# Kernel optimization log

Hardware: AMD Instinct MI355X
Metric: run time of the kernel (lower is better)

The kernel has to match this reference:

```python
import jax, jax.numpy as jnp
import numpy as np

B, LQ, LK, D = 8, 2048, 2048, 128

def setup_inputs() -> dict:
    key = jax.random.key(0)
    k1, k2, k3, k4 = jax.random.split(key, 4)
    return {
        "query": jax.random.normal(k1, (B, LQ, D), dtype=jnp.float32),
        "key": jax.random.normal(k2, (B, LK, D), dtype=jnp.float32),
        "value": jax.random.normal(k3, (B, LK, D), dtype=jnp.float32),
        "scale_factor": jax.random.normal(k4, (B, LQ, LK), dtype=jnp.float32),
    }

def reference(query, key, value, scale_factor):
    # qk: [B, LQ, LK]
    qk = jnp.einsum("bqd,bkd->bqk", query, key)
    probs = jax.nn.softmax(qk * scale_factor, axis=-1)
    # dropout_p = 0.0 -> identity
    return jnp.einsum("bqk,bkd->bqd", probs, value)
```

## Files before the change

### kernel.cpp

```cpp
#include <hip/hip_runtime.h>
#include <hip/hip_bf16.h>


typedef float          f32x4 __attribute__((ext_vector_type(4)));
typedef short          s16x8 __attribute__((ext_vector_type(8)));
typedef unsigned int   u32x4 __attribute__((ext_vector_type(4)));
typedef unsigned short u16x4 __attribute__((ext_vector_type(4)));

#define LOG2E 1.4426950408889634f

__device__ __forceinline__ float fast_exp2(float x) {
#if __has_builtin(__builtin_amdgcn_exp2f)
    return __builtin_amdgcn_exp2f(x);
#else
    return exp2f(x);
#endif
}

__device__ __forceinline__ unsigned short f2bf(float x) {
    return __builtin_bit_cast(unsigned short, __float2bfloat16(x));
}
__device__ __forceinline__ float bf2f(unsigned short u) {
    return __bfloat162float(__builtin_bit_cast(__hip_bfloat16, u));
}

__global__ void prep(const float* __restrict__ q,
                     const float* __restrict__ k,
                     const float* __restrict__ v,
                     unsigned short* __restrict__ qh,
                     unsigned short* __restrict__ ql,
                     unsigned short* __restrict__ kh,
                     unsigned short* __restrict__ kl,
                     unsigned short* __restrict__ vt) {
    __shared__ unsigned short tile[64 * 132];
    const int bb  = blockIdx.x;
    const int tid = threadIdx.x;

    if (bb < 4096) {
        const bool isq = bb < 2048;
        const float* src = isq ? q : k;
        unsigned short* hi = isq ? qh : kh;
        unsigned short* lo = isq ? ql : kl;
        const int i = (isq ? bb : bb - 2048) * 256 + tid;
        const float4 val = ((const float4*)src)[i];
        float f[4] = {val.x, val.y, val.z, val.w};
        u16x4 h, l;
#pragma unroll
        for (int j = 0; j < 4; ++j) {
            unsigned short hb = f2bf(f[j]);
            h[j] = hb;
            l[j] = f2bf(f[j] - bf2f(hb));
        }
        ((u16x4*)hi)[i] = h;
        ((u16x4*)lo)[i] = l;
        return;
    }

    const int tb = bb - 4096;
    const int b  = tb & 7;
    const int k0 = (tb >> 3) * 64;
#pragma unroll
    for (int p = 0; p < 8; ++p) {
        int idx  = p * 256 + tid;
        int kk   = idx >> 5;
        int dblk = idx & 31;
        float4 val = ((const float4*)v)[((b * 2048 + k0 + kk) * 128 + dblk * 4) >> 2];
        u16x4 t4;
        t4[0] = f2bf(val.x); t4[1] = f2bf(val.y);
        t4[2] = f2bf(val.z); t4[3] = f2bf(val.w);
        *(u16x4*)&tile[kk * 132 + dblk * 4] = t4;
    }
    __syncthreads();
#pragma unroll
    for (int p = 0; p < 4; ++p) {
        int idx = p * 256 + tid;
        int d   = idx >> 3;
        int k8  = idx & 7;
        u16x4 a, c;
#pragma unroll
        for (int j = 0; j < 4; ++j) a[j] = tile[(k8 * 8 + j) * 132 + d];
#pragma unroll
        for (int j = 0; j < 4; ++j) c[j] = tile[(k8 * 8 + 4 + j) * 132 + d];
        unsigned short* outp = vt + (b * 128 + d) * 2048 + k0 + k8 * 8;
        *(u16x4*)outp       = a;
        *(u16x4*)(outp + 4) = c;
    }
}

#define KHS 136
#define VTS 72

template <int KSPLIT>
__global__ __launch_bounds__(256, 3)
void flash_fwd(const unsigned short* __restrict__ qh_g,
               const unsigned short* __restrict__ ql_g,
               const unsigned short* __restrict__ kh_g,
               const unsigned short* __restrict__ kl_g,
               const unsigned short* __restrict__ vt_g,
               const float* __restrict__ scale_g,
               float* __restrict__ opart,
               float* __restrict__ mpart,
               float* __restrict__ lpart) {
    __shared__ unsigned short lds_kh[64 * KHS];
    __shared__ unsigned short lds_kl[64 * KHS];
    __shared__ unsigned short lds_vt[128 * VTS];

    const int tid  = threadIdx.x;
    const int wave = tid >> 6;
    const int lane = tid & 63;
    const int c    = lane & 15;
    const int g    = lane >> 4;

    const int bid   = blockIdx.x;
    const int b     = bid & 7;
    const int qt    = (bid >> 3) & 31;
    const int ks    = bid >> 8;
    const int q0    = qt * 64;

    const int PER   = (32 + KSPLIT - 1) / KSPLIT;
    const int kt0   = ks * PER;
    const int NIT   = min(PER, 32 - kt0);
    const int kbase = kt0 * 64;

    const int srow = tid >> 4, sc8 = tid & 15;
    const int sdv  = tid >> 3, sk8 = tid & 7;

    const int rc = 8 * (c >> 2) + (c & 3);

    s16x8 qh[4], ql[4];
    {
        const int qrow = b * 2048 + q0 + wave * 16 + c;
#pragma unroll
        for (int kstep = 0; kstep < 4; ++kstep) {
            int idx = qrow * 16 + kstep * 4 + g;
            qh[kstep] = __builtin_bit_cast(s16x8, ((const u32x4*)qh_g)[idx]);
            ql[kstep] = __builtin_bit_cast(s16x8, ((const u32x4*)ql_g)[idx]);
        }
    }

    f32x4 oacc[8];
#pragma unroll
    for (int t = 0; t < 8; ++t) oacc[t] = (f32x4){0.f, 0.f, 0.f, 0.f};
    float m2 = -INFINITY, ln = 0.f;

    u32x4 pk[4], pl[4], pv[4];
    float4 scn[4];
    const size_t scb = (size_t)(b * 2048 + q0 + wave * 16 + c) * 2048 + 8 * g;

    {
        const int k0 = kbase;
#pragma unroll
        for (int p = 0; p < 4; ++p) {
            int gidx = (b * 2048 + k0 + p * 16 + srow) * 16 + sc8;
            pk[p] = ((const u32x4*)kh_g)[gidx];
            pl[p] = ((const u32x4*)kl_g)[gidx];
            int vidx = (b * 128 + p * 32 + sdv) * 256 + (k0 >> 3) + sk8;
            pv[p] = ((const u32x4*)vt_g)[vidx];
        }
        scn[0] = *(const float4*)&scale_g[scb + k0 + 0];
        scn[1] = *(const float4*)&scale_g[scb + k0 + 32];
        scn[2] = *(const float4*)&scale_g[scb + k0 + 4];
        scn[3] = *(const float4*)&scale_g[scb + k0 + 36];
    }

    for (int kc = 0; kc < NIT; ++kc) {
        const int k0 = kbase + kc * 64;

        __syncthreads();
#pragma unroll
        for (int p = 0; p < 4; ++p) {
            *(u32x4*)&lds_kh[(p * 16 + srow) * KHS + sc8 * 8] = pk[p];
            *(u32x4*)&lds_kl[(p * 16 + srow) * KHS + sc8 * 8] = pl[p];
            *(u32x4*)&lds_vt[(p * 32 + sdv) * VTS + sk8 * 8]  = pv[p];
        }
        __syncthreads();

        float scl[4][4];
#pragma unroll
        for (int t = 0; t < 4; ++t) {
            scl[t][0] = scn[t].x * LOG2E; scl[t][1] = scn[t].y * LOG2E;
            scl[t][2] = scn[t].z * LOG2E; scl[t][3] = scn[t].w * LOG2E;
        }

        if (kc < NIT - 1) {
            const int kn = k0 + 64;
#pragma unroll
            for (int p = 0; p < 4; ++p) {
                int gidx = (b * 2048 + kn + p * 16 + srow) * 16 + sc8;
                pk[p] = ((const u32x4*)kh_g)[gidx];
                pl[p] = ((const u32x4*)kl_g)[gidx];
                int vidx = (b * 128 + p * 32 + sdv) * 256 + (kn >> 3) + sk8;
                pv[p] = ((const u32x4*)vt_g)[vidx];
            }
            scn[0] = *(const float4*)&scale_g[scb + kn + 0];
            scn[1] = *(const float4*)&scale_g[scb + kn + 32];
            scn[2] = *(const float4*)&scale_g[scb + kn + 4];
            scn[3] = *(const float4*)&scale_g[scb + kn + 36];
        }

        f32x4 s[4];
#pragma unroll
        for (int t = 0; t < 4; ++t) s[t] = (f32x4){0.f, 0.f, 0.f, 0.f};
#pragma unroll
        for (int kstep = 0; kstep < 4; ++kstep) {
            const int co = kstep * 32 + g * 8;
            {
                s16x8 bh = *(const s16x8*)&lds_kh[(rc + 0) * KHS + co];
                s16x8 bl = *(const s16x8*)&lds_kl[(rc + 0) * KHS + co];
                s[0] = __builtin_amdgcn_mfma_f32_16x16x32_bf16(bh, qh[kstep], s[0], 0, 0, 0);
                s[0] = __builtin_amdgcn_mfma_f32_16x16x32_bf16(bh, ql[kstep], s[0], 0, 0, 0);
                s[0] = __builtin_amdgcn_mfma_f32_16x16x32_bf16(bl, qh[kstep], s[0], 0, 0, 0);
            }
            {
                s16x8 bh = *(const s16x8*)&lds_kh[(rc + 32) * KHS + co];
                s16x8 bl = *(const s16x8*)&lds_kl[(rc + 32) * KHS + co];
                s[1] = __builtin_amdgcn_mfma_f32_16x16x32_bf16(bh, qh[kstep], s[1], 0, 0, 0);
                s[1] = __builtin_amdgcn_mfma_f32_16x16x32_bf16(bh, ql[kstep], s[1], 0, 0, 0);
                s[1] = __builtin_amdgcn_mfma_f32_16x16x32_bf16(bl, qh[kstep], s[1], 0, 0, 0);
            }
            {
                s16x8 bh = *(const s16x8*)&lds_kh[(rc + 4) * KHS + co];
                s16x8 bl = *(const s16x8*)&lds_kl[(rc + 4) * KHS + co];
                s[2] = __builtin_amdgcn_mfma_f32_16x16x32_bf16(bh, qh[kstep], s[2], 0, 0, 0);
                s[2] = __builtin_amdgcn_mfma_f32_16x16x32_bf16(bh, ql[kstep], s[2], 0, 0, 0);
                s[2] = __builtin_amdgcn_mfma_f32_16x16x32_bf16(bl, qh[kstep], s[2], 0, 0, 0);
            }
            {
                s16x8 bh = *(const s16x8*)&lds_kh[(rc + 36) * KHS + co];
                s16x8 bl = *(const s16x8*)&lds_kl[(rc + 36) * KHS + co];
                s[3] = __builtin_amdgcn_mfma_f32_16x16x32_bf16(bh, qh[kstep], s[3], 0, 0, 0);
                s[3] = __builtin_amdgcn_mfma_f32_16x16x32_bf16(bh, ql[kstep], s[3], 0, 0, 0);
                s[3] = __builtin_amdgcn_mfma_f32_16x16x32_bf16(bl, qh[kstep], s[3], 0, 0, 0);
            }
        }

        float p[4][4];
        float mx = -INFINITY;
#pragma unroll
        for (int t = 0; t < 4; ++t)
#pragma unroll
            for (int r = 0; r < 4; ++r) {
                float v = s[t][r] * scl[t][r];
                p[t][r] = v;
                mx = fmaxf(mx, v);
            }
        mx = fmaxf(mx, __shfl_xor(mx, 16));
        mx = fmaxf(mx, __shfl_xor(mx, 32));
        const float mn = fmaxf(m2, mx);
        const float al = fast_exp2(m2 - mn);
        m2 = mn;
        float rs = 0.f;
#pragma unroll
        for (int t = 0; t < 4; ++t)
#pragma unroll
            for (int r = 0; r < 4; ++r) {
                float pe = fast_exp2(p[t][r] - mn);
                p[t][r] = pe;
                rs += pe;
            }
        rs += __shfl_xor(rs, 16);
        rs += __shfl_xor(rs, 32);
        ln = ln * al + rs;

        float alr[4];
#pragma unroll
        for (int r = 0; r < 4; ++r)
            alr[r] = __shfl(al, (lane & 48) | (g * 4 + r));
#pragma unroll
        for (int t2 = 0; t2 < 8; ++t2)
#pragma unroll
            for (int r = 0; r < 4; ++r) oacc[t2][r] *= alr[r];

        unsigned int w[8];
#pragma unroll
        for (int t = 0; t < 4; ++t)
#pragma unroll
            for (int h = 0; h < 2; ++h)
                w[t * 2 + h] = (unsigned int)f2bf(p[t][2 * h]) |
                               ((unsigned int)f2bf(p[t][2 * h + 1]) << 16);
        u32x4 af0 = {w[0], w[1], w[4], w[5]};
        u32x4 af1 = {w[2], w[3], w[6], w[7]};

        {
            s16x8 a0 = __builtin_bit_cast(s16x8, af0);
#pragma unroll
            for (int t2 = 0; t2 < 8; ++t2) {
                s16x8 bv = *(const s16x8*)&lds_vt[(t2 * 16 + c) * VTS + g * 8];
                oacc[t2] = __builtin_amdgcn_mfma_f32_16x16x32_bf16(a0, bv, oacc[t2], 0, 0, 0);
            }
            s16x8 a1 = __builtin_bit_cast(s16x8, af1);
#pragma unroll
            for (int t2 = 0; t2 < 8; ++t2) {
                s16x8 bv = *(const s16x8*)&lds_vt[(t2 * 16 + c) * VTS + 32 + g * 8];
                oacc[t2] = __builtin_amdgcn_mfma_f32_16x16x32_bf16(a1, bv, oacc[t2], 0, 0, 0);
            }
        }
    }

    {
        const int rowb = (ks * 8 + b) * 2048 + q0 + wave * 16;
#pragma unroll
        for (int t2 = 0; t2 < 8; ++t2)
#pragma unroll
            for (int r = 0; r < 4; ++r)
                opart[(size_t)(rowb + g * 4 + r) * 128 + t2 * 16 + c] = oacc[t2][r];
        if (g == 0) {
            mpart[rowb + c] = m2;
            lpart[rowb + c] = ln;
        }
    }
}

template <int KSPLIT>
__global__ void merge_parts(const float* __restrict__ opart,
                            const float* __restrict__ mpart,
                            const float* __restrict__ lpart,
                            float* __restrict__ out) {
    const int row = blockIdx.x;
    const int d   = threadIdx.x;
    float m[KSPLIT], l[KSPLIT];
    float M = -INFINITY;
#pragma unroll
    for (int i = 0; i < KSPLIT; ++i) {
        m[i] = mpart[i * 16384 + row];
        l[i] = lpart[i * 16384 + row];
        M = fmaxf(M, m[i]);
    }
    float denom = 0.f, acc = 0.f;
    const size_t base = (size_t)row * 128 + d;
#pragma unroll
    for (int i = 0; i < KSPLIT; ++i) {
        const float a = fast_exp2(m[i] - M);
        denom += a * l[i];
        acc   += a * opart[(size_t)i * 16384 * 128 + base];
    }
    out[base] = acc / denom;
}

extern "C" void kernel_launch(void* const* d_in, const int* in_sizes, int n_in,
                              void* d_out, int out_size, void* d_ws, size_t ws_size,
                              hipStream_t stream) {
    const float* q  = (const float*)d_in[0];
    const float* k  = (const float*)d_in[1];
    const float* v  = (const float*)d_in[2];
    const float* sc = (const float*)d_in[3];
    float* out = (float*)d_out;

    char* ws = (char*)d_ws;
    const size_t MB = 1024 * 1024;
    unsigned short* qh = (unsigned short*)(ws);
    unsigned short* ql = (unsigned short*)(ws + 4 * MB);
    unsigned short* kh = (unsigned short*)(ws + 8 * MB);
    unsigned short* kl = (unsigned short*)(ws + 12 * MB);
    unsigned short* vt = (unsigned short*)(ws + 16 * MB);

    prep<<<4352, 256, 0, stream>>>(q, k, v, qh, ql, kh, kl, vt);

    const size_t need3 = 44 * MB + 512 * 1024;
    if (ws_size >= need3) {
        float* opart = (float*)(ws + 20 * MB);
        float* mpart = (float*)(ws + 44 * MB);
        float* lpart = (float*)(ws + 44 * MB + 256 * 1024);
        flash_fwd<3><<<768, 256, 0, stream>>>(qh, ql, kh, kl, vt, sc, opart, mpart, lpart);
        merge_parts<3><<<16384, 128, 0, stream>>>(opart, mpart, lpart, out);
    } else {
        float* opart = (float*)(ws + 20 * MB);
        float* mpart = (float*)(ws + 36 * MB);
        float* lpart = (float*)(ws + 36 * MB + 128 * 1024);
        flash_fwd<2><<<512, 256, 0, stream>>>(qh, ql, kh, kl, vt, sc, opart, mpart, lpart);
        merge_parts<2><<<16384, 128, 0, stream>>>(opart, mpart, lpart, out);
    }
}
```

Before: 310.9 us.

## Pre-swizzle K/V into MFMA fragment order and double-buffer 32-key LDS tiles

The prep kernel now writes K (hi/lo bf16 split) and transposed V as 32-key tiles already laid out in MFMA fragment order. The attention kernel can then copy each tile into LDS contiguously and read it with unit-stride, unpadded fragment loads. The main loop now processes two 32-key tiles per iteration with A/B LDS double buffering and one barrier per tile, so global loads overlap compute. The cost is halving the keys per softmax step, which doubles the online-softmax rescale and reduction work. The loop also assumes each split has an even tile count.

Result: faster. 248.9 us (-20.0%).

```diff
diff --git a/kernel.cpp b/kernel.cpp
--- a/kernel.cpp
+++ b/kernel.cpp
@@ -29,20 +29,16 @@
                      const float* __restrict__ v,
                      unsigned short* __restrict__ qh,
                      unsigned short* __restrict__ ql,
-                     unsigned short* __restrict__ kh,
-                     unsigned short* __restrict__ kl,
-                     unsigned short* __restrict__ vt) {
-    __shared__ unsigned short tile[64 * 132];
+                     unsigned short* __restrict__ khf,
+                     unsigned short* __restrict__ klf,
+                     unsigned short* __restrict__ vtf) {
+    __shared__ __attribute__((aligned(16))) float smem[2 * 32 * 132];
     const int bb  = blockIdx.x;
     const int tid = threadIdx.x;
 
-    if (bb < 4096) {
-        const bool isq = bb < 2048;
-        const float* src = isq ? q : k;
-        unsigned short* hi = isq ? qh : kh;
-        unsigned short* lo = isq ? ql : kl;
-        const int i = (isq ? bb : bb - 2048) * 256 + tid;
-        const float4 val = ((const float4*)src)[i];
+    if (bb < 2048) {
+        const int i = bb * 256 + tid;
+        const float4 val = ((const float4*)q)[i];
         float f[4] = {val.x, val.y, val.z, val.w};
         u16x4 h, l;
 #pragma unroll
@@ -51,84 +47,175 @@
             h[j] = hb;
             l[j] = f2bf(f[j] - bf2f(hb));
         }
-        ((u16x4*)hi)[i] = h;
-        ((u16x4*)lo)[i] = l;
+        ((u16x4*)qh)[i] = h;
+        ((u16x4*)ql)[i] = l;
         return;
     }
 
-    const int tb = bb - 4096;
-    const int b  = tb & 7;
-    const int k0 = (tb >> 3) * 64;
-#pragma unroll
-    for (int p = 0; p < 8; ++p) {
-        int idx  = p * 256 + tid;
-        int kk   = idx >> 5;
-        int dblk = idx & 31;
-        float4 val = ((const float4*)v)[((b * 2048 + k0 + kk) * 128 + dblk * 4) >> 2];
-        u16x4 t4;
-        t4[0] = f2bf(val.x); t4[1] = f2bf(val.y);
-        t4[2] = f2bf(val.z); t4[3] = f2bf(val.w);
-        *(u16x4*)&tile[kk * 132 + dblk * 4] = t4;
-    }
-    __syncthreads();
+    float* kt = smem;
+    float* vt = smem + 32 * 132;
+    const int blk = bb - 2048;
+    const int b   = blk >> 6;
+    const int T   = blk & 63;
+    const size_t rbase = ((size_t)b * 2048 + T * 32) * 128;
 #pragma unroll
     for (int p = 0; p < 4; ++p) {
         int idx = p * 256 + tid;
-        int d   = idx >> 3;
-        int k8  = idx & 7;
-        u16x4 a, c;
-#pragma unroll
-        for (int j = 0; j < 4; ++j) a[j] = tile[(k8 * 8 + j) * 132 + d];
-#pragma unroll
-        for (int j = 0; j < 4; ++j) c[j] = tile[(k8 * 8 + 4 + j) * 132 + d];
-        unsigned short* outp = vt + (b * 128 + d) * 2048 + k0 + k8 * 8;
-        *(u16x4*)outp       = a;
-        *(u16x4*)(outp + 4) = c;
-    }
-}
-
-#define KHS 136
-#define VTS 72
+        int row = idx >> 5, c4 = (idx & 31) * 4;
+        *(float4*)&kt[row * 132 + c4] = *(const float4*)&k[rbase + row * 128 + c4];
+        *(float4*)&vt[row * 132 + c4] = *(const float4*)&v[rbase + row * 128 + c4];
+    }
+    __syncthreads();
+    const size_t obase = (size_t)(b * 64 + T) * 4096;
+#pragma unroll
+    for (int p = 0; p < 2; ++p) {
+        const int item = p * 256 + tid;
+        const int f = item >> 6, lane = item & 63;
+        const int c = lane & 15, g = lane >> 4;
+        {
+            const int t = f >> 2, ks2 = f & 3;
+            const int row = 8 * (c >> 2) + (c & 3) + 4 * t;
+            const int col = ks2 * 32 + g * 8;
+            float vals[8];
+            *(float4*)&vals[0] = *(const float4*)&kt[row * 132 + col];
+            *(float4*)&vals[4] = *(const float4*)&kt[row * 132 + col + 4];
+            unsigned int wh[4], wl[4];
+#pragma unroll
+            for (int j = 0; j < 4; ++j) {
+                unsigned short h0 = f2bf(vals[2 * j]), h1 = f2bf(vals[2 * j + 1]);
+                unsigned short l0 = f2bf(vals[2 * j]     - bf2f(h0));
+                unsigned short l1 = f2bf(vals[2 * j + 1] - bf2f(h1));
+                wh[j] = (unsigned int)h0 | ((unsigned int)h1 << 16);
+                wl[j] = (unsigned int)l0 | ((unsigned int)l1 << 16);
+            }
+            *(u32x4*)&khf[obase + f * 512 + lane * 8] = (u32x4){wh[0], wh[1], wh[2], wh[3]};
+            *(u32x4*)&klf[obase + f * 512 + lane * 8] = (u32x4){wl[0], wl[1], wl[2], wl[3]};
+        }
+        {
+            unsigned int wv[4];
+#pragma unroll
+            for (int j = 0; j < 4; ++j) {
+                unsigned short a0 = f2bf(vt[(g * 8 + 2 * j)     * 132 + f * 16 + c]);
+                unsigned short a1 = f2bf(vt[(g * 8 + 2 * j + 1) * 132 + f * 16 + c]);
+                wv[j] = (unsigned int)a0 | ((unsigned int)a1 << 16);
+            }
+            *(u32x4*)&vtf[obase + f * 512 + lane * 8] = (u32x4){wv[0], wv[1], wv[2], wv[3]};
+        }
+    }
+}
+
+
+__device__ __forceinline__ void compute_tile(
+    const unsigned short* lkh, const unsigned short* lkl,
+    const unsigned short* lvt,
+    const s16x8 qh[4], const s16x8 ql[4],
+    const float4 sv0, const float4 sv1,
+    f32x4 oacc[8], float& m2, float& ln,
+    const int fb, const int lane) {
+    const int g = lane >> 4;
+    f32x4 s[2];
+    s[0] = (f32x4){0.f, 0.f, 0.f, 0.f};
+    s[1] = (f32x4){0.f, 0.f, 0.f, 0.f};
+#pragma unroll
+    for (int kstep = 0; kstep < 4; ++kstep) {
+#pragma unroll
+        for (int t = 0; t < 2; ++t) {
+            const int off = (t * 4 + kstep) * 512 + fb;
+            s16x8 bh = *(const s16x8*)&lkh[off];
+            s16x8 bl = *(const s16x8*)&lkl[off];
+            s[t] = __builtin_amdgcn_mfma_f32_16x16x32_bf16(bh, qh[kstep], s[t], 0, 0, 0);
+            s[t] = __builtin_amdgcn_mfma_f32_16x16x32_bf16(bh, ql[kstep], s[t], 0, 0, 0);
+            s[t] = __builtin_amdgcn_mfma_f32_16x16x32_bf16(bl, qh[kstep], s[t], 0, 0, 0);
+        }
+    }
+    float p[2][4];
+    p[0][0] = s[0][0] * (sv0.x * LOG2E); p[0][1] = s[0][1] * (sv0.y * LOG2E);
+    p[0][2] = s[0][2] * (sv0.z * LOG2E); p[0][3] = s[0][3] * (sv0.w * LOG2E);
+    p[1][0] = s[1][0] * (sv1.x * LOG2E); p[1][1] = s[1][1] * (sv1.y * LOG2E);
+    p[1][2] = s[1][2] * (sv1.z * LOG2E); p[1][3] = s[1][3] * (sv1.w * LOG2E);
+    float mx = -INFINITY;
+#pragma unroll
+    for (int t = 0; t < 2; ++t)
+#pragma unroll
+        for (int r = 0; r < 4; ++r) mx = fmaxf(mx, p[t][r]);
+    mx = fmaxf(mx, __shfl_xor(mx, 16));
+    mx = fmaxf(mx, __shfl_xor(mx, 32));
+    const float mn = fmaxf(m2, mx);
+    const float al = fast_exp2(m2 - mn);
+    m2 = mn;
+    float rs = 0.f;
+#pragma unroll
+    for (int t = 0; t < 2; ++t)
+#pragma unroll
+        for (int r = 0; r < 4; ++r) {
+            float pe = fast_exp2(p[t][r] - mn);
+            p[t][r] = pe;
+            rs += pe;
+        }
+    rs += __shfl_xor(rs, 16);
+    rs += __shfl_xor(rs, 32);
+    ln = ln * al + rs;
+    float alr[4];
+#pragma unroll
+    for (int r = 0; r < 4; ++r)
+        alr[r] = __shfl(al, (lane & 48) | (g * 4 + r));
+#pragma unroll
+    for (int t2 = 0; t2 < 8; ++t2)
+#pragma unroll
+        for (int r = 0; r < 4; ++r) oacc[t2][r] *= alr[r];
+    unsigned int w0 = (unsigned int)f2bf(p[0][0]) | ((unsigned int)f2bf(p[0][1]) << 16);
+    unsigned int w1 = (unsigned int)f2bf(p[0][2]) | ((unsigned int)f2bf(p[0][3]) << 16);
+    unsigned int w2 = (unsigned int)f2bf(p[1][0]) | ((unsigned int)f2bf(p[1][1]) << 16);
+    unsigned int w3 = (unsigned int)f2bf(p[1][2]) | ((unsigned int)f2bf(p[1][3]) << 16);
+    u32x4 afu = {w0, w1, w2, w3};
+    s16x8 af = __builtin_bit_cast(s16x8, afu);
+#pragma unroll
+    for (int t2 = 0; t2 < 8; ++t2) {
+        s16x8 bv = *(const s16x8*)&lvt[t2 * 512 + fb];
+        oacc[t2] = __builtin_amdgcn_mfma_f32_16x16x32_bf16(af, bv, oacc[t2], 0, 0, 0);
+    }
+}
 
 template <int KSPLIT>
 __global__ __launch_bounds__(256, 3)
 void flash_fwd(const unsigned short* __restrict__ qh_g,
                const unsigned short* __restrict__ ql_g,
-               const unsigned short* __restrict__ kh_g,
-               const unsigned short* __restrict__ kl_g,
-               const unsigned short* __restrict__ vt_g,
+               const unsigned short* __restrict__ khf_g,
+               const unsigned short* __restrict__ klf_g,
+               const unsigned short* __restrict__ vtf_g,
                const float* __restrict__ scale_g,
                float* __restrict__ opart,
                float* __restrict__ mpart,
                float* __restrict__ lpart) {
-    __shared__ unsigned short lds_kh[64 * KHS];
-    __shared__ unsigned short lds_kl[64 * KHS];
-    __shared__ unsigned short lds_vt[128 * VTS];
+    __shared__ __attribute__((aligned(16))) unsigned short khA[4096];
+    __shared__ __attribute__((aligned(16))) unsigned short klA[4096];
+    __shared__ __attribute__((aligned(16))) unsigned short vtA[4096];
+    __shared__ __attribute__((aligned(16))) unsigned short khB[4096];
+    __shared__ __attribute__((aligned(16))) unsigned short klB[4096];
+    __shared__ __attribute__((aligned(16))) unsigned short vtB[4096];
 
     const int tid  = threadIdx.x;
     const int wave = tid >> 6;
     const int lane = tid & 63;
     const int c    = lane & 15;
-    const int g    = lane >> 4;
-
-    const int bid   = blockIdx.x;
-    const int b     = bid & 7;
-    const int qt    = (bid >> 3) & 31;
-    const int ks    = bid >> 8;
-    const int q0    = qt * 64;
-
-    const int PER   = (32 + KSPLIT - 1) / KSPLIT;
-    const int kt0   = ks * PER;
-    const int NIT   = min(PER, 32 - kt0);
-    const int kbase = kt0 * 64;
-
-    const int srow = tid >> 4, sc8 = tid & 15;
-    const int sdv  = tid >> 3, sk8 = tid & 7;
-
-    const int rc = 8 * (c >> 2) + (c & 3);
+    const int fb   = lane * 8;
+
+    const int bid = blockIdx.x;
+    const int b   = bid & 7;
+    const int qt  = (bid >> 3) & 31;
+    const int ks  = bid >> 8;
+    const int q0  = qt * 64;
+
+    const int TILES = 64;
+    const int PER   = (TILES + KSPLIT - 1) / KSPLIT;
+    const int T0    = ks * PER;
+    const int NIT   = min(PER, TILES - T0);
+
+    const size_t fbase = (size_t)b * 64 * 4096;
 
     s16x8 qh[4], ql[4];
     {
+        const int g    = lane >> 4;
         const int qrow = b * 2048 + q0 + wave * 16 + c;
 #pragma unroll
         for (int kstep = 0; kstep < 4; ++kstep) {
@@ -138,166 +225,59 @@
         }
     }
 
+    const size_t scb = (size_t)(b * 2048 + q0 + wave * 16 + c) * 2048 + 8 * (lane >> 4);
+
     f32x4 oacc[8];
 #pragma unroll
     for (int t = 0; t < 8; ++t) oacc[t] = (f32x4){0.f, 0.f, 0.f, 0.f};
     float m2 = -INFINITY, ln = 0.f;
 
-    u32x4 pk[4], pl[4], pv[4];
-    float4 scn[4];
-    const size_t scb = (size_t)(b * 2048 + q0 + wave * 16 + c) * 2048 + 8 * g;
+    const int o0 = tid * 8, o1 = (256 + tid) * 8;
+
+    u32x4 rg[6];
+    auto loadT = [&](int T) {
+        const size_t tb = fbase + (size_t)T * 4096;
+        rg[0] = *(const u32x4*)&khf_g[tb + o0];
+        rg[1] = *(const u32x4*)&khf_g[tb + o1];
+        rg[2] = *(const u32x4*)&klf_g[tb + o0];
+        rg[3] = *(const u32x4*)&klf_g[tb + o1];
+        rg[4] = *(const u32x4*)&vtf_g[tb + o0];
+        rg[5] = *(const u32x4*)&vtf_g[tb + o1];
+    };
+    auto writeT = [&](unsigned short* lkh, unsigned short* lkl, unsigned short* lvt) {
+        *(u32x4*)&lkh[o0] = rg[0];  *(u32x4*)&lkh[o1] = rg[1];
+        *(u32x4*)&lkl[o0] = rg[2];  *(u32x4*)&lkl[o1] = rg[3];
+        *(u32x4*)&lvt[o0] = rg[4];  *(u32x4*)&lvt[o1] = rg[5];
+    };
+
+    loadT(T0);
+    writeT(khA, klA, vtA);
+    float4 sA0 = *(const float4*)&scale_g[scb + (size_t)T0 * 32];
+    float4 sA1 = *(const float4*)&scale_g[scb + (size_t)T0 * 32 + 4];
+
+    for (int it = 0; it < NIT; it += 2) {
+        const int T = T0 + it;
+        __syncthreads();
+        loadT(T + 1);
+        float4 sB0 = *(const float4*)&scale_g[scb + (size_t)(T + 1) * 32];
+        float4 sB1 = *(const float4*)&scale_g[scb + (size_t)(T + 1) * 32 + 4];
+        __builtin_amdgcn_sched_barrier(0);
+        compute_tile(khA, klA, vtA, qh, ql, sA0, sA1, oacc, m2, ln, fb, lane);
+        writeT(khB, klB, vtB);
+        __syncthreads();
+        const bool more = (it + 2 < NIT);
+        if (more) {
+            loadT(T + 2);
+            sA0 = *(const float4*)&scale_g[scb + (size_t)(T + 2) * 32];
+            sA1 = *(const float4*)&scale_g[scb + (size_t)(T + 2) * 32 + 4];
+            __builtin_amdgcn_sched_barrier(0);
+        }
+        compute_tile(khB, klB, vtB, qh, ql, sB0, sB1, oacc, m2, ln, fb, lane);
+        if (more) writeT(khA, klA, vtA);
+    }
 
     {
-        const int k0 = kbase;
-#pragma unroll
-        for (int p = 0; p < 4; ++p) {
-            int gidx = (b * 2048 + k0 + p * 16 + srow) * 16 + sc8;
-            pk[p] = ((const u32x4*)kh_g)[gidx];
-            pl[p] = ((const u32x4*)kl_g)[gidx];
-            int vidx = (b * 128 + p * 32 + sdv) * 256 + (k0 >> 3) + sk8;
-            pv[p] = ((const u32x4*)vt_g)[vidx];
-        }
-        scn[0] = *(const float4*)&scale_g[scb + k0 + 0];
-        scn[1] = *(const float4*)&scale_g[scb + k0 + 32];
-        scn[2] = *(const float4*)&scale_g[scb + k0 + 4];
-        scn[3] = *(const float4*)&scale_g[scb + k0 + 36];
-    }
-
-    for (int kc = 0; kc < NIT; ++kc) {
-        const int k0 = kbase + kc * 64;
-
-        __syncthreads();
-#pragma unroll
-        for (int p = 0; p < 4; ++p) {
-            *(u32x4*)&lds_kh[(p * 16 + srow) * KHS + sc8 * 8] = pk[p];
-            *(u32x4*)&lds_kl[(p * 16 + srow) * KHS + sc8 * 8] = pl[p];
-            *(u32x4*)&lds_vt[(p * 32 + sdv) * VTS + sk8 * 8]  = pv[p];
-        }
-        __syncthreads();
-
-        float scl[4][4];
-#pragma unroll
-        for (int t = 0; t < 4; ++t) {
-            scl[t][0] = scn[t].x * LOG2E; scl[t][1] = scn[t].y * LOG2E;
-            scl[t][2] = scn[t].z * LOG2E; scl[t][3] = scn[t].w * LOG2E;
-        }
-
-        if (kc < NIT - 1) {
-            const int kn = k0 + 64;
-#pragma unroll
-            for (int p = 0; p < 4; ++p) {
-                int gidx = (b * 2048 + kn + p * 16 + srow) * 16 + sc8;
-                pk[p] = ((const u32x4*)kh_g)[gidx];
-                pl[p] = ((const u32x4*)kl_g)[gidx];
-                int vidx = (b * 128 + p * 32 + sdv) * 256 + (kn >> 3) + sk8;
-                pv[p] = ((const u32x4*)vt_g)[vidx];
-            }
-            scn[0] = *(const float4*)&scale_g[scb + kn + 0];
-            scn[1] = *(const float4*)&scale_g[scb + kn + 32];
-            scn[2] = *(const float4*)&scale_g[scb + kn + 4];
-            scn[3] = *(const float4*)&scale_g[scb + kn + 36];
-        }
-
-        f32x4 s[4];
-#pragma unroll
-        for (int t = 0; t < 4; ++t) s[t] = (f32x4){0.f, 0.f, 0.f, 0.f};
-#pragma unroll
-        for (int kstep = 0; kstep < 4; ++kstep) {
-            const int co = kstep * 32 + g * 8;
-            {
-                s16x8 bh = *(const s16x8*)&lds_kh[(rc + 0) * KHS + co];
-                s16x8 bl = *(const s16x8*)&lds_kl[(rc + 0) * KHS + co];
-                s[0] = __builtin_amdgcn_mfma_f32_16x16x32_bf16(bh, qh[kstep], s[0], 0, 0, 0);
-                s[0] = __builtin_amdgcn_mfma_f32_16x16x32_bf16(bh, ql[kstep], s[0], 0, 0, 0);
-                s[0] = __builtin_amdgcn_mfma_f32_16x16x32_bf16(bl, qh[kstep], s[0], 0, 0, 0);
-            }
-            {
-                s16x8 bh = *(const s16x8*)&lds_kh[(rc + 32) * KHS + co];
-                s16x8 bl = *(const s16x8*)&lds_kl[(rc + 32) * KHS + co];
-                s[1] = __builtin_amdgcn_mfma_f32_16x16x32_bf16(bh, qh[kstep], s[1], 0, 0, 0);
-                s[1] = __builtin_amdgcn_mfma_f32_16x16x32_bf16(bh, ql[kstep], s[1], 0, 0, 0);
-                s[1] = __builtin_amdgcn_mfma_f32_16x16x32_bf16(bl, qh[kstep], s[1], 0, 0, 0);
-            }
-            {
-                s16x8 bh = *(const s16x8*)&lds_kh[(rc + 4) * KHS + co];
-                s16x8 bl = *(const s16x8*)&lds_kl[(rc + 4) * KHS + co];
-                s[2] = __builtin_amdgcn_mfma_f32_16x16x32_bf16(bh, qh[kstep], s[2], 0, 0, 0);
-                s[2] = __builtin_amdgcn_mfma_f32_16x16x32_bf16(bh, ql[kstep], s[2], 0, 0, 0);
-                s[2] = __builtin_amdgcn_mfma_f32_16x16x32_bf16(bl, qh[kstep], s[2], 0, 0, 0);
-            }
-            {
-                s16x8 bh = *(const s16x8*)&lds_kh[(rc + 36) * KHS + co];
-                s16x8 bl = *(const s16x8*)&lds_kl[(rc + 36) * KHS + co];
-                s[3] = __builtin_amdgcn_mfma_f32_16x16x32_bf16(bh, qh[kstep], s[3], 0, 0, 0);
-                s[3] = __builtin_amdgcn_mfma_f32_16x16x32_bf16(bh, ql[kstep], s[3], 0, 0, 0);
-                s[3] = __builtin_amdgcn_mfma_f32_16x16x32_bf16(bl, qh[kstep], s[3], 0, 0, 0);
-            }
-        }
-
-        float p[4][4];
-        float mx = -INFINITY;
-#pragma unroll
-        for (int t = 0; t < 4; ++t)
-#pragma unroll
-            for (int r = 0; r < 4; ++r) {
-                float v = s[t][r] * scl[t][r];
-                p[t][r] = v;
-                mx = fmaxf(mx, v);
-            }
-        mx = fmaxf(mx, __shfl_xor(mx, 16));
-        mx = fmaxf(mx, __shfl_xor(mx, 32));
-        const float mn = fmaxf(m2, mx);
-        const float al = fast_exp2(m2 - mn);
-        m2 = mn;
-        float rs = 0.f;
-#pragma unroll
-        for (int t = 0; t < 4; ++t)
-#pragma unroll
-            for (int r = 0; r < 4; ++r) {
-                float pe = fast_exp2(p[t][r] - mn);
-                p[t][r] = pe;
-                rs += pe;
-            }
-        rs += __shfl_xor(rs, 16);
-        rs += __shfl_xor(rs, 32);
-        ln = ln * al + rs;
-
-        float alr[4];
-#pragma unroll
-        for (int r = 0; r < 4; ++r)
-            alr[r] = __shfl(al, (lane & 48) | (g * 4 + r));
-#pragma unroll
-        for (int t2 = 0; t2 < 8; ++t2)
-#pragma unroll
-            for (int r = 0; r < 4; ++r) oacc[t2][r] *= alr[r];
-
-        unsigned int w[8];
-#pragma unroll
-        for (int t = 0; t < 4; ++t)
-#pragma unroll
-            for (int h = 0; h < 2; ++h)
-                w[t * 2 + h] = (unsigned int)f2bf(p[t][2 * h]) |
-                               ((unsigned int)f2bf(p[t][2 * h + 1]) << 16);
-        u32x4 af0 = {w[0], w[1], w[4], w[5]};
-        u32x4 af1 = {w[2], w[3], w[6], w[7]};
-
-        {
-            s16x8 a0 = __builtin_bit_cast(s16x8, af0);
-#pragma unroll
-            for (int t2 = 0; t2 < 8; ++t2) {
-                s16x8 bv = *(const s16x8*)&lds_vt[(t2 * 16 + c) * VTS + g * 8];
-                oacc[t2] = __builtin_amdgcn_mfma_f32_16x16x32_bf16(a0, bv, oacc[t2], 0, 0, 0);
-            }
-            s16x8 a1 = __builtin_bit_cast(s16x8, af1);
-#pragma unroll
-            for (int t2 = 0; t2 < 8; ++t2) {
-                s16x8 bv = *(const s16x8*)&lds_vt[(t2 * 16 + c) * VTS + 32 + g * 8];
-                oacc[t2] = __builtin_amdgcn_mfma_f32_16x16x32_bf16(a1, bv, oacc[t2], 0, 0, 0);
-            }
-        }
-    }
-
-    {
+        const int g    = lane >> 4;
         const int rowb = (ks * 8 + b) * 2048 + q0 + wave * 16;
 #pragma unroll
         for (int t2 = 0; t2 < 8; ++t2)
@@ -348,26 +328,26 @@
 
     char* ws = (char*)d_ws;
     const size_t MB = 1024 * 1024;
-    unsigned short* qh = (unsigned short*)(ws);
-    unsigned short* ql = (unsigned short*)(ws + 4 * MB);
-    unsigned short* kh = (unsigned short*)(ws + 8 * MB);
-    unsigned short* kl = (unsigned short*)(ws + 12 * MB);
-    unsigned short* vt = (unsigned short*)(ws + 16 * MB);
-
-    prep<<<4352, 256, 0, stream>>>(q, k, v, qh, ql, kh, kl, vt);
+    unsigned short* qh  = (unsigned short*)(ws);
+    unsigned short* ql  = (unsigned short*)(ws + 4 * MB);
+    unsigned short* khf = (unsigned short*)(ws + 8 * MB);
+    unsigned short* klf = (unsigned short*)(ws + 12 * MB);
+    unsigned short* vtf = (unsigned short*)(ws + 16 * MB);
+
+    prep<<<2560, 256, 0, stream>>>(q, k, v, qh, ql, khf, klf, vtf);
 
     const size_t need3 = 44 * MB + 512 * 1024;
     if (ws_size >= need3) {
         float* opart = (float*)(ws + 20 * MB);
         float* mpart = (float*)(ws + 44 * MB);
         float* lpart = (float*)(ws + 44 * MB + 256 * 1024);
-        flash_fwd<3><<<768, 256, 0, stream>>>(qh, ql, kh, kl, vt, sc, opart, mpart, lpart);
+        flash_fwd<3><<<768, 256, 0, stream>>>(qh, ql, khf, klf, vtf, sc, opart, mpart, lpart);
         merge_parts<3><<<16384, 128, 0, stream>>>(opart, mpart, lpart, out);
     } else {
         float* opart = (float*)(ws + 20 * MB);
         float* mpart = (float*)(ws + 36 * MB);
         float* lpart = (float*)(ws + 36 * MB + 128 * 1024);
-        flash_fwd<2><<<512, 256, 0, stream>>>(qh, ql, kh, kl, vt, sc, opart, mpart, lpart);
+        flash_fwd<2><<<512, 256, 0, stream>>>(qh, ql, khf, klf, vtf, sc, opart, mpart, lpart);
         merge_parts<2><<<16384, 128, 0, stream>>>(opart, mpart, lpart, out);
     }
 }
```
